# Optimization experiments

Measured on AMD Instinct MI355X. Metric: run time of the kernel, lower is better.

The kernel has to match this reference:

```python
import jax, jax.numpy as jnp
import numpy as np

B, D, E, N = 2048, 4096, 512, 8192
BN_EPS = 1e-5
COS_EPS = 1e-8


def setup_inputs() -> dict:
    key = jax.random.key(0)
    k1, k2, k3, k4, k5 = jax.random.split(key, 5)
    vf = jax.random.normal(k1, (B, D), dtype=jnp.float32)
    p_wfs = jax.random.normal(k2, (B, D), dtype=jnp.float32)
    n_wfs = jax.random.normal(k3, (N, E), dtype=jnp.float32)
    # BatchNorm1d(4096) affine params (default init gamma=1, beta=0; use random-ish gamma for generality)
    gamma = jnp.ones((D,), dtype=jnp.float32)
    beta = jnp.zeros((D,), dtype=jnp.float32)
    # Linear(D -> E)
    lim = 1.0 / np.sqrt(D)
    W = jax.random.uniform(k4, (E, D), dtype=jnp.float32, minval=-lim, maxval=lim)
    b = jax.random.uniform(k5, (E,), dtype=jnp.float32, minval=-lim, maxval=lim)
    return {"vf": vf, "p_wfs": p_wfs, "n_wfs": n_wfs, "gamma": gamma, "beta": beta, "W": W, "b": b}


def _row_normalize(x, eps=COS_EPS):
    nrm = jnp.sqrt(jnp.sum(x * x, axis=-1, keepdims=True))
    return x / jnp.maximum(nrm, eps)


def reference(vf, p_wfs, n_wfs, gamma, beta, W, b):
    # BatchNorm1d in training mode: batch mean / biased variance over the batch dim
    mean = jnp.mean(vf, axis=0)
    var = jnp.mean((vf - mean) ** 2, axis=0)
    vfn = (vf - mean) * (gamma / jnp.sqrt(var + BN_EPS)) + beta  # [B, D]

    # Linear + ReLU embedding
    emb = jax.nn.relu(vfn @ W.T + b)  # [B, E]

    # p_e: row-wise cosine(normed vf, p_wfs) -> [B]
    p_e = jnp.sum(_row_normalize(vfn) * _row_normalize(p_wfs), axis=-1)

    # n_e: cosine(emb[v], n_wfs[n]) for all v,n -> one normalized GEMM [B, N]
    n_e = _row_normalize(emb) @ _row_normalize(n_wfs).T

    n_neg = n_wfs.shape[0]
    n_e_stack = n_e.reshape(-1, 1)                      # [B*N, 1]
    p_e_stack = jnp.repeat(p_e, n_neg).reshape(-1, 1)   # [B*N, 1], p_e[v] repeated N times
    return (n_e_stack, p_e_stack)
```

## Files before the change

kernel.cpp:

```cpp
#include <hip/hip_runtime.h>
#include <stdint.h>
#include <stddef.h>

#define B_ 2048
#define D_ 4096
#define E_ 512
#define N_ 8192
#define SPLITK 4

typedef unsigned short ushort_t;
typedef __attribute__((ext_vector_type(8))) short short8;
typedef __attribute__((ext_vector_type(4))) float floatx4;
typedef __attribute__((ext_vector_type(4))) unsigned short ushort4_t;

__device__ __forceinline__ void async_load16(const void* g, void* l) {
  __builtin_amdgcn_global_load_lds((__attribute__((address_space(1))) void*)(g),
                                   (__attribute__((address_space(3))) void*)(l), 16, 0, 0);
}

__device__ __forceinline__ ushort_t f2bf(float f) {
  unsigned int u = __float_as_uint(f);
  unsigned int r = (u + 0x7fffu + ((u >> 16) & 1u)) >> 16;
  return (ushort_t)r;
}
__device__ __forceinline__ float bf2f(ushort_t h) {
  return __uint_as_float(((unsigned int)h) << 16);
}

__global__ __launch_bounds__(256) void bn_partial(const float* __restrict__ vf,
                                                  float* __restrict__ psum,
                                                  float* __restrict__ psq) {
  int d4 = blockIdx.x * 256 + threadIdx.x;
  int chunk = blockIdx.y;
  floatx4 s = {0.f, 0.f, 0.f, 0.f}, q = {0.f, 0.f, 0.f, 0.f};
  int r0 = chunk * 32;
  for (int r = r0; r < r0 + 32; ++r) {
    floatx4 v = ((const floatx4*)(vf + (size_t)r * D_))[d4];
    s += v; q += v * v;
  }
  ((floatx4*)(psum + (size_t)chunk * D_))[d4] = s;
  ((floatx4*)(psq  + (size_t)chunk * D_))[d4] = q;
}

__global__ __launch_bounds__(256) void bn_finalize(const float* __restrict__ psum,
                                                   const float* __restrict__ psq,
                                                   const float* __restrict__ gamma,
                                                   const float* __restrict__ beta,
                                                   float* __restrict__ scale,
                                                   float* __restrict__ shift) {
  int d4 = blockIdx.x * 256 + threadIdx.x;
  floatx4 s = {0.f, 0.f, 0.f, 0.f}, q = {0.f, 0.f, 0.f, 0.f};
  for (int c = 0; c < 64; ++c) {
    s += ((const floatx4*)(psum + (size_t)c * D_))[d4];
    q += ((const floatx4*)(psq  + (size_t)c * D_))[d4];
  }
  floatx4 g = ((const floatx4*)gamma)[d4];
  floatx4 bt = ((const floatx4*)beta)[d4];
  floatx4 sc, sh;
#pragma unroll
  for (int j = 0; j < 4; ++j) {
    float mean = s[j] * (1.0f / B_);
    float var  = q[j] * (1.0f / B_) - mean * mean;
    float scj  = g[j] * rsqrtf(var + 1e-5f);
    sc[j] = scj;
    sh[j] = bt[j] - mean * scj;
  }
  ((floatx4*)scale)[d4] = sc;
  ((floatx4*)shift)[d4] = sh;
}

__global__ __launch_bounds__(256) void pe_cast(const float* __restrict__ vf,
                                               const float* __restrict__ p,
                                               const float* __restrict__ scale,
                                               const float* __restrict__ shift,
                                               ushort_t* __restrict__ vfn,
                                               float* __restrict__ pe) {
  int wv = threadIdx.x >> 6, l = threadIdx.x & 63;
  int v = blockIdx.x * 4 + wv;
  const floatx4* vf4 = (const floatx4*)(vf + (size_t)v * D_);
  const floatx4* p4  = (const floatx4*)(p  + (size_t)v * D_);
  const floatx4* sc4 = (const floatx4*)scale;
  const floatx4* sh4 = (const floatx4*)shift;
  ushort_t* vrow = vfn + (size_t)v * D_;
  float sd = 0.f, sa = 0.f, sb = 0.f;
#pragma unroll 4
  for (int k = 0; k < 16; ++k) {
    int i = l + 64 * k;
    floatx4 x = vf4[i], y = p4[i], s = sc4[i], t = sh4[i];
    ushort4_t o;
#pragma unroll
    for (int j = 0; j < 4; ++j) {
      float xn = x[j] * s[j] + t[j];
      o[j] = f2bf(xn);
      sd += xn * y[j]; sa += xn * xn; sb += y[j] * y[j];
    }
    *(ushort4_t*)(vrow + i * 4) = o;
  }
  for (int off = 32; off; off >>= 1) {
    sd += __shfl_down(sd, off); sa += __shfl_down(sa, off); sb += __shfl_down(sb, off);
  }
  if (l == 0) {
    float na = fmaxf(sqrtf(sa), 1e-8f), nb = fmaxf(sqrtf(sb), 1e-8f);
    pe[v] = sd / (na * nb);
  }
}

__global__ __launch_bounds__(256) void prep_kernel(const float* __restrict__ W,
                                                   const float* __restrict__ nw,
                                                   ushort_t* __restrict__ wb,
                                                   ushort_t* __restrict__ nwb,
                                                   float* __restrict__ inv_nw) {
  int bid = blockIdx.x;
  if (bid < 2048) {
    size_t i = ((size_t)bid * 256 + threadIdx.x) * 4;
    floatx4 x = *(const floatx4*)(W + i);
    ushort4_t o;
#pragma unroll
    for (int j = 0; j < 4; ++j) o[j] = f2bf(x[j]);
    *(ushort4_t*)(wb + i) = o;
  } else {
    int wv = threadIdx.x >> 6, l = threadIdx.x & 63;
    int n = (bid - 2048) * 4 + wv;
    const floatx4* src = (const floatx4*)(nw + (size_t)n * E_);
    ushort4_t* dst = (ushort4_t*)(nwb + (size_t)n * E_);
    float s = 0.f;
#pragma unroll
    for (int k = 0; k < 2; ++k) {
      floatx4 x = src[l + 64 * k];
      ushort4_t o;
#pragma unroll
      for (int j = 0; j < 4; ++j) { o[j] = f2bf(x[j]); s += x[j] * x[j]; }
      dst[l + 64 * k] = o;
    }
    for (int off = 32; off; off >>= 1) s += __shfl_down(s, off);
    if (l == 0) inv_nw[n] = 1.f / fmaxf(sqrtf(s), 1e-8f);
  }
}

template <int BM, int BN, int BK, int WCOLS, int MT, int NT>
__device__ __forceinline__ void gemm_core(const ushort_t* __restrict__ A,
                                          const ushort_t* __restrict__ Bt, int K,
                                          int kb, int ke, int bm0, int bn0,
                                          ushort_t* As, ushort_t* Bs,
                                          floatx4 (&acc)[MT][NT]) {
  const int tid = threadIdx.x, w = tid >> 6, l = tid & 63;
  constexpr int ISS_A = BM * BK / 2048;
  constexpr int ISS_B = BN * BK / 2048;
  const int wr = w / WCOLS, wc = w % WCOLS;
  const int m16 = l & 15, q = l >> 4;

  for (int k0 = kb; k0 < ke; k0 += BK) {
#pragma unroll
    for (int i = 0; i < ISS_A; ++i) {
      int e = i * 2048 + tid * 8;
      int row = e / BK, col = e % BK;
      async_load16(A + (size_t)(bm0 + row) * K + (k0 + col), &As[i * 2048 + w * 512]);
    }
#pragma unroll
    for (int i = 0; i < ISS_B; ++i) {
      int e = i * 2048 + tid * 8;
      int row = e / BK, col = e % BK;
      async_load16(Bt + (size_t)(bn0 + row) * K + (k0 + col), &Bs[i * 2048 + w * 512]);
    }
    __syncthreads();
#pragma unroll
    for (int kc = 0; kc < BK / 32; ++kc) {
      short8 af[MT], bf[NT];
#pragma unroll
      for (int i = 0; i < MT; ++i)
        af[i] = *(const short8*)&As[(wr * (MT * 16) + i * 16 + m16) * BK + kc * 32 + q * 8];
#pragma unroll
      for (int j = 0; j < NT; ++j)
        bf[j] = *(const short8*)&Bs[(wc * (NT * 16) + j * 16 + m16) * BK + kc * 32 + q * 8];
#pragma unroll
      for (int i = 0; i < MT; ++i)
#pragma unroll
        for (int j = 0; j < NT; ++j)
          acc[i][j] = __builtin_amdgcn_mfma_f32_16x16x32_bf16(af[i], bf[j], acc[i][j], 0, 0, 0);
    }
    __syncthreads();
  }
}

__global__ __launch_bounds__(256, 2) void gemm1_splitk(const ushort_t* __restrict__ A,
                                                       const ushort_t* __restrict__ Bt,
                                                       float* __restrict__ partial) {
  __shared__ __align__(16) ushort_t As[128 * 64];
  __shared__ __align__(16) ushort_t Bs[64 * 64];
  floatx4 acc[4][2] = {};
  int bm0 = blockIdx.y * 128, bn0 = blockIdx.x * 64, s = blockIdx.z;
  int kb = s * (D_ / SPLITK);
  gemm_core<128, 64, 64, 2, 4, 2>(A, Bt, D_, kb, kb + D_ / SPLITK, bm0, bn0, As, Bs, acc);
  int tid = threadIdx.x, w = tid >> 6, l = tid & 63, m16 = l & 15, q = l >> 4;
  int wr = w >> 1, wc = w & 1;
  float* out = partial + (size_t)s * B_ * E_;
#pragma unroll
  for (int i = 0; i < 4; ++i)
#pragma unroll
    for (int j = 0; j < 2; ++j) {
      int col = bn0 + wc * 32 + j * 16 + m16;
#pragma unroll
      for (int r = 0; r < 4; ++r) {
        int row = bm0 + wr * 64 + i * 16 + q * 4 + r;
        out[(size_t)row * E_ + col] = acc[i][j][r];
      }
    }
}

__global__ __launch_bounds__(256) void gemm1_reduce(const float* __restrict__ partial,
                                                    const float* __restrict__ bias,
                                                    ushort_t* __restrict__ emb,
                                                    float* __restrict__ inv_emb) {
  int wv = threadIdx.x >> 6, l = threadIdx.x & 63;
  int row = blockIdx.x * 4 + wv;
  float sumsq = 0.f;
#pragma unroll
  for (int k = 0; k < 2; ++k) {
    int i = l + 64 * k;
    floatx4 v = {0.f, 0.f, 0.f, 0.f};
#pragma unroll
    for (int s = 0; s < SPLITK; ++s)
      v += ((const floatx4*)(partial + (size_t)s * B_ * E_ + (size_t)row * E_))[i];
    floatx4 bb = ((const floatx4*)bias)[i];
    ushort4_t o;
#pragma unroll
    for (int j = 0; j < 4; ++j) {
      float f = fmaxf(v[j] + bb[j], 0.f);
      o[j] = f2bf(f);
      float fb = bf2f(o[j]);
      sumsq += fb * fb;
    }
    ((ushort4_t*)(emb + (size_t)row * E_))[i] = o;
  }
  for (int off = 32; off; off >>= 1) sumsq += __shfl_down(sumsq, off);
  if (l == 0) inv_emb[row] = 1.f / fmaxf(sqrtf(sumsq), 1e-8f);
}

__global__ __launch_bounds__(256, 2) void gemm2_kernel(const ushort_t* __restrict__ A,
                                                       const ushort_t* __restrict__ Bt,
                                                       const float* __restrict__ inv_a,
                                                       const float* __restrict__ inv_b,
                                                       const float* __restrict__ pe,
                                                       float* __restrict__ out) {
  __shared__ __align__(16) ushort_t As[128 * 64];
  __shared__ __align__(16) ushort_t Bs[256 * 64];
  floatx4 acc[4][8] = {};
  int bm0 = blockIdx.y * 128, bn0 = blockIdx.x * 256;
  gemm_core<128, 256, 64, 2, 4, 8>(A, Bt, E_, 0, E_, bm0, bn0, As, Bs, acc);
  int tid = threadIdx.x, w = tid >> 6, l = tid & 63, m16 = l & 15, q = l >> 4;
  int wr = w >> 1, wc = w & 1;
  float* out2 = out + (size_t)B_ * N_;
  float ibv[8];
#pragma unroll
  for (int j = 0; j < 8; ++j) ibv[j] = inv_b[bn0 + wc * 128 + j * 16 + m16];
#pragma unroll
  for (int i = 0; i < 4; ++i)
#pragma unroll
    for (int r = 0; r < 4; ++r) {
      int row = bm0 + wr * 64 + i * 16 + q * 4 + r;
      float ia = inv_a[row];
      float pv = pe[row];
      size_t base = (size_t)row * N_ + bn0 + wc * 128 + m16;
#pragma unroll
      for (int j = 0; j < 8; ++j) {
        out[base + j * 16]  = acc[i][j][r] * ia * ibv[j];
        out2[base + j * 16] = pv;
      }
    }
}

extern "C" void kernel_launch(void* const* d_in, const int* in_sizes, int n_in,
                              void* d_out, int out_size, void* d_ws, size_t ws_size,
                              hipStream_t stream) {
  (void)in_sizes; (void)n_in; (void)out_size; (void)ws_size;
  const float* vf    = (const float*)d_in[0];
  const float* p_wfs = (const float*)d_in[1];
  const float* n_wfs = (const float*)d_in[2];
  const float* gamma = (const float*)d_in[3];
  const float* beta  = (const float*)d_in[4];
  const float* W     = (const float*)d_in[5];
  const float* bias  = (const float*)d_in[6];
  float* out = (float*)d_out;

  char* ws = (char*)d_ws;
  float* psum    = (float*)ws;  ws += (size_t)64 * D_ * 4;
  float* psq     = (float*)ws;  ws += (size_t)64 * D_ * 4;
  float* scale   = (float*)ws;  ws += (size_t)D_ * 4;
  float* shift   = (float*)ws;  ws += (size_t)D_ * 4;
  float* pe      = (float*)ws;  ws += (size_t)B_ * 4;
  float* inv_nw  = (float*)ws;  ws += (size_t)N_ * 4;
  float* inv_emb = (float*)ws;  ws += (size_t)B_ * 4;
  float* partial = (float*)ws;  ws += (size_t)SPLITK * B_ * E_ * 4;
  ushort_t* vfn  = (ushort_t*)ws;  ws += (size_t)B_ * D_ * 2;
  ushort_t* wb   = (ushort_t*)ws;  ws += (size_t)E_ * D_ * 2;
  ushort_t* nwb  = (ushort_t*)ws;  ws += (size_t)N_ * E_ * 2;
  ushort_t* emb  = (ushort_t*)ws;  ws += (size_t)B_ * E_ * 2;

  bn_partial<<<dim3(D_ / 1024, 64), 256, 0, stream>>>(vf, psum, psq);
  bn_finalize<<<D_ / 1024, 256, 0, stream>>>(psum, psq, gamma, beta, scale, shift);
  pe_cast<<<B_ / 4, 256, 0, stream>>>(vf, p_wfs, scale, shift, vfn, pe);
  prep_kernel<<<2048 + N_ / 4, 256, 0, stream>>>(W, n_wfs, wb, nwb, inv_nw);
  gemm1_splitk<<<dim3(E_ / 64, B_ / 128, SPLITK), 256, 0, stream>>>(vfn, wb, partial);
  gemm1_reduce<<<B_ / 4, 256, 0, stream>>>(partial, bias, emb, inv_emb);
  gemm2_kernel<<<dim3(N_ / 256, B_ / 128), 256, 0, stream>>>(emb, nwb, inv_emb, inv_nw, pe, out);
}
```

Measured before the change: 281.4 us.

## Merge BN finalize into prep kernel and interleave p_e stores with GEMM2 main loop

Merges the BN finalize and the weight/negative-bank cast kernels into one launch, which removes one kernel launch. GEMM2 is rewritten with 128x128 tiles and an inlined K loop. The repeated p_e output stores are spread across the K iterations so the large write stream overlaps with MFMA work instead of all landing in the epilogue. The smaller tile doubles the grid and lowers per-block register use, but it also cuts data reuse per tile.

```diff
diff --git a/kernel.cpp b/kernel.cpp
--- a/kernel.cpp
+++ b/kernel.cpp
@@ -42,31 +42,62 @@
   ((floatx4*)(psq  + (size_t)chunk * D_))[d4] = q;
 }
 
-__global__ __launch_bounds__(256) void bn_finalize(const float* __restrict__ psum,
-                                                   const float* __restrict__ psq,
-                                                   const float* __restrict__ gamma,
-                                                   const float* __restrict__ beta,
-                                                   float* __restrict__ scale,
-                                                   float* __restrict__ shift) {
-  int d4 = blockIdx.x * 256 + threadIdx.x;
-  floatx4 s = {0.f, 0.f, 0.f, 0.f}, q = {0.f, 0.f, 0.f, 0.f};
-  for (int c = 0; c < 64; ++c) {
-    s += ((const floatx4*)(psum + (size_t)c * D_))[d4];
-    q += ((const floatx4*)(psq  + (size_t)c * D_))[d4];
-  }
-  floatx4 g = ((const floatx4*)gamma)[d4];
-  floatx4 bt = ((const floatx4*)beta)[d4];
-  floatx4 sc, sh;
-#pragma unroll
-  for (int j = 0; j < 4; ++j) {
-    float mean = s[j] * (1.0f / B_);
-    float var  = q[j] * (1.0f / B_) - mean * mean;
-    float scj  = g[j] * rsqrtf(var + 1e-5f);
-    sc[j] = scj;
-    sh[j] = bt[j] - mean * scj;
-  }
-  ((floatx4*)scale)[d4] = sc;
-  ((floatx4*)shift)[d4] = sh;
+__global__ __launch_bounds__(256) void prep_all(const float* __restrict__ psum,
+                                                const float* __restrict__ psq,
+                                                const float* __restrict__ gamma,
+                                                const float* __restrict__ beta,
+                                                const float* __restrict__ W,
+                                                const float* __restrict__ nw,
+                                                float* __restrict__ scale,
+                                                float* __restrict__ shift,
+                                                ushort_t* __restrict__ wb,
+                                                ushort_t* __restrict__ nwb,
+                                                float* __restrict__ inv_nw) {
+  int bid = blockIdx.x;
+  if (bid < 4) {
+    int d4 = bid * 256 + threadIdx.x;
+    floatx4 s = {0.f, 0.f, 0.f, 0.f}, q = {0.f, 0.f, 0.f, 0.f};
+    for (int c = 0; c < 64; ++c) {
+      s += ((const floatx4*)(psum + (size_t)c * D_))[d4];
+      q += ((const floatx4*)(psq  + (size_t)c * D_))[d4];
+    }
+    floatx4 g = ((const floatx4*)gamma)[d4];
+    floatx4 bt = ((const floatx4*)beta)[d4];
+    floatx4 sc, sh;
+#pragma unroll
+    for (int j = 0; j < 4; ++j) {
+      float mean = s[j] * (1.0f / B_);
+      float var  = q[j] * (1.0f / B_) - mean * mean;
+      float scj  = g[j] * rsqrtf(var + 1e-5f);
+      sc[j] = scj;
+      sh[j] = bt[j] - mean * scj;
+    }
+    ((floatx4*)scale)[d4] = sc;
+    ((floatx4*)shift)[d4] = sh;
+  } else if (bid < 2052) {
+    size_t i = ((size_t)(bid - 4) * 256 + threadIdx.x) * 4;
+    floatx4 x = *(const floatx4*)(W + i);
+    ushort4_t o;
+#pragma unroll
+    for (int j = 0; j < 4; ++j) o[j] = f2bf(x[j]);
+    *(ushort4_t*)(wb + i) = o;
+  } else {
+    int wv = threadIdx.x >> 6, l = threadIdx.x & 63;
+    int n = (bid - 2052) * 4 + wv;
+    const floatx4* src = (const floatx4*)(nw + (size_t)n * E_);
+    ushort4_t* dst = (ushort4_t*)(nwb + (size_t)n * E_);
+    float s = 0.f;
+#pragma unroll
+    for (int k = 0; k < 2; ++k) {
+      floatx4 x = src[l + 64 * k];
+      ushort4_t o;
+#pragma unroll
+      for (int j = 0; j < 4; ++j) { o[j] = f2bf(x[j]); s += x[j] * x[j]; }
+      dst[l + 64 * k] = o;
+    }
+    for (int off = 32; off; off >>= 1) s += __shfl_down(s, off);
+    if (l == 0) inv_nw[n] = 1.f / fmaxf(sqrtf(s), 1e-8f);
+  }
 }
 
 __global__ __launch_bounds__(256) void pe_cast(const float* __restrict__ vf,
@@ -105,38 +136,6 @@
   }
 }
 
-__global__ __launch_bounds__(256) void prep_kernel(const float* __restrict__ W,
-                                                   const float* __restrict__ nw,
-                                                   ushort_t* __restrict__ wb,
-                                                   ushort_t* __restrict__ nwb,
-                                                   float* __restrict__ inv_nw) {
-  int bid = blockIdx.x;
-  if (bid < 2048) {
-    size_t i = ((size_t)bid * 256 + threadIdx.x) * 4;
-    floatx4 x = *(const floatx4*)(W + i);
-    ushort4_t o;
-#pragma unroll
-    for (int j = 0; j < 4; ++j) o[j] = f2bf(x[j]);
-    *(ushort4_t*)(wb + i) = o;
-  } else {
-    int wv = threadIdx.x >> 6, l = threadIdx.x & 63;
-    int n = (bid - 2048) * 4 + wv;
-    const floatx4* src = (const floatx4*)(nw + (size_t)n * E_);
-    ushort4_t* dst = (ushort4_t*)(nwb + (size_t)n * E_);
-    float s = 0.f;
-#pragma unroll
-    for (int k = 0; k < 2; ++k) {
-      floatx4 x = src[l + 64 * k];
-      ushort4_t o;
-#pragma unroll
-      for (int j = 0; j < 4; ++j) { o[j] = f2bf(x[j]); s += x[j] * x[j]; }
-      dst[l + 64 * k] = o;
-    }
-    for (int off = 32; off; off >>= 1) s += __shfl_down(s, off);
-    if (l == 0) inv_nw[n] = 1.f / fmaxf(sqrtf(s), 1e-8f);
-  }
-}
-
 template <int BM, int BN, int BK, int WCOLS, int MT, int NT>
 __device__ __forceinline__ void gemm_core(const ushort_t* __restrict__ A,
                                           const ushort_t* __restrict__ Bt, int K,
@@ -243,29 +242,73 @@
                                                        const float* __restrict__ pe,
                                                        float* __restrict__ out) {
   __shared__ __align__(16) ushort_t As[128 * 64];
-  __shared__ __align__(16) ushort_t Bs[256 * 64];
-  floatx4 acc[4][8] = {};
-  int bm0 = blockIdx.y * 128, bn0 = blockIdx.x * 256;
-  gemm_core<128, 256, 64, 2, 4, 8>(A, Bt, E_, 0, E_, bm0, bn0, As, Bs, acc);
-  int tid = threadIdx.x, w = tid >> 6, l = tid & 63, m16 = l & 15, q = l >> 4;
-  int wr = w >> 1, wc = w & 1;
-  float* out2 = out + (size_t)B_ * N_;
-  float ibv[8];
-#pragma unroll
-  for (int j = 0; j < 8; ++j) ibv[j] = inv_b[bn0 + wc * 128 + j * 16 + m16];
+  __shared__ __align__(16) ushort_t Bs[128 * 64];
+  floatx4 acc[4][4] = {};
+  const int tid = threadIdx.x, w = tid >> 6, l = tid & 63;
+  const int m16 = l & 15, q = l >> 4;
+  const int wr = w >> 1, wc = w & 1;
+  const int bm0 = blockIdx.y * 128, bn0 = blockIdx.x * 128;
+
+  float pv[4][4];
+#pragma unroll
+  for (int i = 0; i < 4; ++i)
+#pragma unroll
+    for (int r = 0; r < 4; ++r)
+      pv[i][r] = pe[bm0 + wr * 64 + i * 16 + q * 4 + r];
+  float* out2lane = out + (size_t)B_ * N_ + bn0 + wc * 64 + m16;
+
+#pragma unroll
+  for (int it = 0; it < E_ / 64; ++it) {
+    int k0 = it * 64;
+#pragma unroll
+    for (int i = 0; i < 4; ++i) {
+      int e = i * 2048 + tid * 8;
+      async_load16(A + (size_t)(bm0 + e / 64) * E_ + (k0 + e % 64), &As[i * 2048 + w * 512]);
+    }
+#pragma unroll
+    for (int i = 0; i < 4; ++i) {
+      int e = i * 2048 + tid * 8;
+      async_load16(Bt + (size_t)(bn0 + e / 64) * E_ + (k0 + e % 64), &Bs[i * 2048 + w * 512]);
+    }
+    __syncthreads();
+#pragma unroll
+    for (int t = 0; t < 8; ++t) {
+      int idx = it * 8 + t;
+      int i = idx >> 4, r = (idx >> 2) & 3, j = idx & 3;
+      int row = bm0 + wr * 64 + i * 16 + q * 4 + r;
+      out2lane[(size_t)row * N_ + j * 16] = pv[i][r];
+    }
+#pragma unroll
+    for (int kc = 0; kc < 2; ++kc) {
+      short8 af[4], bf[4];
+#pragma unroll
+      for (int i = 0; i < 4; ++i)
+        af[i] = *(const short8*)&As[(wr * 64 + i * 16 + m16) * 64 + kc * 32 + q * 8];
+#pragma unroll
+      for (int j = 0; j < 4; ++j)
+        bf[j] = *(const short8*)&Bs[(wc * 64 + j * 16 + m16) * 64 + kc * 32 + q * 8];
+#pragma unroll
+      for (int i = 0; i < 4; ++i)
+#pragma unroll
+        for (int j = 0; j < 4; ++j)
+          acc[i][j] = __builtin_amdgcn_mfma_f32_16x16x32_bf16(af[i], bf[j], acc[i][j], 0, 0, 0);
+    }
+    __syncthreads();
+  }
+
+  float ibv[4];
+#pragma unroll
+  for (int j = 0; j < 4; ++j) ibv[j] = inv_b[bn0 + wc * 64 + j * 16 + m16];
 #pragma unroll
   for (int i = 0; i < 4; ++i)
 #pragma unroll
     for (int r = 0; r < 4; ++r) {
       int row = bm0 + wr * 64 + i * 16 + q * 4 + r;
       float ia = inv_a[row];
-      float pv = pe[row];
-      size_t base = (size_t)row * N_ + bn0 + wc * 128 + m16;
-#pragma unroll
-      for (int j = 0; j < 8; ++j) {
-        out[base + j * 16]  = acc[i][j][r] * ia * ibv[j];
-        out2[base + j * 16] = pv;
-      }
+      size_t base = (size_t)row * N_ + bn0 + wc * 64 + m16;
+#pragma unroll
+      for (int j = 0; j < 4; ++j)
+        out[base + j * 16] = acc[i][j][r] * ia * ibv[j];
     }
 }
 
@@ -297,10 +340,10 @@
   ushort_t* emb  = (ushort_t*)ws;  ws += (size_t)B_ * E_ * 2;
 
   bn_partial<<<dim3(D_ / 1024, 64), 256, 0, stream>>>(vf, psum, psq);
-  bn_finalize<<<D_ / 1024, 256, 0, stream>>>(psum, psq, gamma, beta, scale, shift);
+  prep_all<<<4 + 2048 + N_ / 4, 256, 0, stream>>>(psum, psq, gamma, beta, W, n_wfs,
+                                                  scale, shift, wb, nwb, inv_nw);
   pe_cast<<<B_ / 4, 256, 0, stream>>>(vf, p_wfs, scale, shift, vfn, pe);
-  prep_kernel<<<2048 + N_ / 4, 256, 0, stream>>>(W, n_wfs, wb, nwb, inv_nw);
   gemm1_splitk<<<dim3(E_ / 64, B_ / 128, SPLITK), 256, 0, stream>>>(vfn, wb, partial);
   gemm1_reduce<<<B_ / 4, 256, 0, stream>>>(partial, bias, emb, inv_emb);
-  gemm2_kernel<<<dim3(N_ / 256, B_ / 128), 256, 0, stream>>>(emb, nwb, inv_emb, inv_nw, pe, out);
-}
+  gemm2_kernel<<<dim3(N_ / 128, B_ / 128), 256, 0, stream>>>(emb, nwb, inv_emb, inv_nw, pe, out);
+}
```

After: 272.2 us. 1.03x faster.
